# Kernel optimization log

Measured on AMD Instinct MI355X. Metric: run time of the kernel, lower is better.

## Reference

```python
import jax, jax.numpy as jnp
import numpy as np

N_NODES = 100000
N_EDGES = 1600000
HID = 64
EDGE_DIM = 32
N_LAYERS = 3
BN_EPS = 1e-5


def setup_inputs() -> dict:
    key = jax.random.key(0)
    ks = jax.random.split(key, 8)
    x = jax.random.normal(ks[0], (N_NODES, HID), dtype=jnp.float32)
    edge_index = jax.random.randint(ks[1], (2, N_EDGES), 0, N_NODES, dtype=jnp.int32)
    edge_attr = jax.random.normal(ks[2], (N_EDGES, EDGE_DIM), dtype=jnp.float32)
    s = 0.1  # small init scale for numerical stability
    We = jax.random.normal(ks[3], (N_LAYERS, EDGE_DIM, HID), dtype=jnp.float32) * s
    be = jnp.zeros((N_LAYERS, HID), jnp.float32)
    W1 = jax.random.normal(ks[4], (N_LAYERS, HID, HID), dtype=jnp.float32) * s
    b1 = jnp.zeros((N_LAYERS, HID), jnp.float32)
    W2 = jax.random.normal(ks[5], (N_LAYERS, HID, HID), dtype=jnp.float32) * s
    b2 = jnp.zeros((N_LAYERS, HID), jnp.float32)
    gamma = jnp.ones((N_LAYERS, HID), jnp.float32)
    beta = jnp.zeros((N_LAYERS, HID), jnp.float32)
    Wout = jax.random.normal(ks[6], (HID, HID), dtype=jnp.float32) * s
    bout = jnp.zeros((HID,), jnp.float32)
    return {"x": x, "edge_index": edge_index, "edge_attr": edge_attr,
            "We": We, "be": be, "W1": W1, "b1": b1, "W2": W2, "b2": b2,
            "gamma": gamma, "beta": beta, "Wout": Wout, "bout": bout}


def _forward(x, edge_index, edge_attr, We, be, W1, b1, W2, b2, gamma, beta, Wout, bout):
    src = edge_index[0]  # x_j (source of message)
    dst = edge_index[1]  # aggregation target
    n = x.shape[0]
    for i in range(N_LAYERS):
        # GINEConv: message = relu(x_j + lin_edge(edge_attr)); scatter-add to dst
        e = edge_attr @ We[i] + be[i]                      # [E, H]
        m = jax.nn.relu(x[src] + e)                        # [E, H] (dominant traffic)
        agg = jax.ops.segment_sum(m, dst, num_segments=n)  # [N, H]
        h = x + agg                                        # (1 + eps)*x, eps = 0
        # 2-layer MLP
        h = jax.nn.relu(h @ W1[i] + b1[i]) @ W2[i] + b2[i]
        # BatchNorm1d (training mode: batch statistics, biased variance)
        mean = jnp.mean(h, axis=0)
        var = jnp.var(h, axis=0)
        h = (h - mean) * jax.lax.rsqrt(var + BN_EPS) * gamma[i] + beta[i]
        x = jax.nn.relu(h)
    return x @ Wout + bout


def reference(x, edge_index, edge_attr, We, be, W1, b1, W2, b2, gamma, beta, Wout, bout):
    return _forward(x, edge_index, edge_attr, We, be, W1, b1, W2, b2, gamma, beta, Wout, bout)
```

## Files before the change

kernel.cpp:

```cpp
#include <hip/hip_runtime.h>
#include <stdint.h>

#define N_NODES 100000
#define N_EDGES 1600000
#define HID 64
#define EDIM 32
#define BN_EPS 1e-5f

#define SCAN_CHUNK 1024
#define NB_SCAN ((N_NODES + SCAN_CHUNK - 1) / SCAN_CHUNK)

#define G_NODES 16

__global__ __launch_bounds__(256) void hist_kernel(
    const int* __restrict__ dst, int* __restrict__ cnt)
{
    int i = (int)(blockIdx.x * blockDim.x + threadIdx.x);
    const int stride = (int)(gridDim.x * blockDim.x);
    for (; i < N_EDGES; i += stride) atomicAdd(&cnt[dst[i]], 1);
}

__global__ __launch_bounds__(256) void scan1_kernel(
    const int* __restrict__ cnt, int* __restrict__ bsum)
{
    __shared__ int s[256];
    const int b = (int)blockIdx.x, t = (int)threadIdx.x;
    const int base = b * SCAN_CHUNK + t * 4;
    int sum = 0;
#pragma unroll
    for (int k = 0; k < 4; ++k) {
        int idx = base + k;
        if (idx < N_NODES) sum += cnt[idx];
    }
    s[t] = sum;
    __syncthreads();
    for (int off = 128; off > 0; off >>= 1) {
        if (t < off) s[t] += s[t + off];
        __syncthreads();
    }
    if (t == 0) bsum[b] = s[0];
}

__global__ __launch_bounds__(128) void scan2_kernel(
    const int* __restrict__ bsum, int* __restrict__ bofs, int* __restrict__ row_ptr)
{
    __shared__ int s[128];
    const int t = (int)threadIdx.x;
    const int v = (t < NB_SCAN) ? bsum[t] : 0;
    s[t] = v;
    __syncthreads();
    for (int off = 1; off < 128; off <<= 1) {
        int add = (t >= off) ? s[t - off] : 0;
        __syncthreads();
        s[t] += add;
        __syncthreads();
    }
    if (t < NB_SCAN) bofs[t] = s[t] - v;
    if (t == NB_SCAN - 1) row_ptr[N_NODES] = s[t];
}

__global__ __launch_bounds__(256) void scan3_kernel(
    const int* __restrict__ cnt, const int* __restrict__ bofs,
    int* __restrict__ row_ptr, int* __restrict__ pos)
{
    __shared__ int s[256];
    const int b = (int)blockIdx.x, t = (int)threadIdx.x;
    const int base = b * SCAN_CHUNK + t * 4;
    int v[4];
    int sum = 0;
#pragma unroll
    for (int k = 0; k < 4; ++k) {
        int idx = base + k;
        v[k] = (idx < N_NODES) ? cnt[idx] : 0;
        sum += v[k];
    }
    s[t] = sum;
    __syncthreads();
    for (int off = 1; off < 256; off <<= 1) {
        int add = (t >= off) ? s[t - off] : 0;
        __syncthreads();
        s[t] += add;
        __syncthreads();
    }
    int run = s[t] - sum + bofs[b];
#pragma unroll
    for (int k = 0; k < 4; ++k) {
        int idx = base + k;
        if (idx < N_NODES) {
            row_ptr[idx] = run;
            pos[idx] = run;
            run += v[k];
        }
    }
}

__global__ __launch_bounds__(256) void scatter_kernel(
    const int* __restrict__ src, const int* __restrict__ dst,
    int* __restrict__ pos, int* __restrict__ perm_e, int* __restrict__ perm_src)
{
    int i = (int)(blockIdx.x * blockDim.x + threadIdx.x);
    const int stride = (int)(gridDim.x * blockDim.x);
    for (; i < N_EDGES; i += stride) {
        const int d = dst[i];
        const int p = atomicAdd(&pos[d], 1);
        perm_e[p] = i;
        perm_src[p] = src[i];
    }
}

__global__ __launch_bounds__(256) void permute_attr_kernel(
    const float* __restrict__ eattr, const int* __restrict__ perm_e,
    float* __restrict__ outp)
{
    const int total = N_EDGES * 8;
    int i = (int)(blockIdx.x * blockDim.x + threadIdx.x);
    const int stride = (int)(gridDim.x * blockDim.x);
    for (; i < total; i += stride) {
        const int row = i >> 3, part = i & 7;
        ((float4*)outp)[i] =
            ((const float4*)eattr)[(size_t)(unsigned)perm_e[row] * 8 + part];
    }
}

template<bool LINEAR>
__global__ __launch_bounds__(256, 4) void gather_kernel(
    const float* __restrict__ x, const float* __restrict__ attr,
    const int* __restrict__ row_ptr, const int* __restrict__ perm_e,
    const int* __restrict__ perm_src,
    const float* __restrict__ We, const float* __restrict__ be,
    float* __restrict__ agg)
{
    const int tid  = (int)threadIdx.x;
    const int lane = tid & 63;
    const int w    = __builtin_amdgcn_readfirstlane(tid >> 6);
    const int node_lo = (int)blockIdx.x * G_NODES + 4 * w;

    int rpv[5];
#pragma unroll
    for (int i = 0; i < 5; ++i) {
        int n = node_lo + i;
        n = (n < N_NODES) ? n : N_NODES;
        rpv[i] = __builtin_amdgcn_readfirstlane(row_ptr[n]);
    }
    const int F0 = rpv[0], rp1 = rpv[1], rp2 = rpv[2], rp3 = rpv[3], F1 = rpv[4];

    float a = 0.0f, sn1 = 0.0f, sn2 = 0.0f, sn3 = 0.0f;

    if (F0 < F1) {
        const int FL = F1 - 1;

        float pf_prev;
        {
            int gl = F0 + lane; if (gl > FL) gl = FL;
            size_t row = LINEAR ? (size_t)gl : (size_t)(unsigned)perm_e[gl];
            pf_prev = attr[row * EDIM];
        }

        float wv[EDIM];
#pragma unroll
        for (int k = 0; k < EDIM; ++k) wv[k] = We[k * HID + lane];
        const float bias = be[lane];

        int jA = F0;
        int jB = F0 + 1; if (jB > FL) jB = FL;
        int jC = F0 + 2; if (jC > FL) jC = FL;
        const int s0 = perm_src[jA];
        const int s1 = perm_src[jB];
        int sN = perm_src[jC];
        float xq0 = x[(size_t)(unsigned)s0 * HID + lane];
        float xq1 = x[(size_t)(unsigned)s1 * HID + lane];

        for (int gb = F0; gb < F1; gb += 64) {
            const int gend = (gb + 64 < F1) ? gb + 64 : F1;

            float pf = 0.0f;
            if (gb + 64 < F1) {
                int gl = gb + 64 + lane; if (gl > FL) gl = FL;
                size_t row = LINEAR ? (size_t)gl : (size_t)(unsigned)perm_e[gl];
                pf = attr[row * EDIM];
            }

#pragma unroll 2
            for (int j = gb; j < gend; ++j) {
                const float xq2 = x[(size_t)(unsigned)sN * HID + lane];
                int j3 = j + 3; if (j3 > FL) j3 = FL;
                sN = perm_src[j3];

                size_t row = LINEAR ? (size_t)j : (size_t)(unsigned)perm_e[j];
                const float4* ap = (const float4*)(attr + row * EDIM);

                float e0 = bias, e1 = 0.0f, e2 = 0.0f, e3 = 0.0f;
#pragma unroll
                for (int k = 0; k < 8; ++k) {
                    const float4 q = ap[k];
                    e0 = fmaf(q.x, wv[4 * k + 0], e0);
                    e1 = fmaf(q.y, wv[4 * k + 1], e1);
                    e2 = fmaf(q.z, wv[4 * k + 2], e2);
                    e3 = fmaf(q.w, wv[4 * k + 3], e3);
                }
                a += fmaxf(xq0 + ((e0 + e1) + (e2 + e3)), 0.0f);
                xq0 = xq1; xq1 = xq2;

                if (j + 1 == rp1) sn1 = a;
                if (j + 1 == rp2) sn2 = a;
                if (j + 1 == rp3) sn3 = a;
            }

            asm volatile("" :: "v"(pf_prev));
            pf_prev = pf;
        }
        asm volatile("" :: "v"(pf_prev));
    }

    float r[4];
    r[0] = sn1;
    r[1] = sn2 - sn1;
    r[2] = sn3 - sn2;
    r[3] = a - sn3;
#pragma unroll
    for (int q = 0; q < 4; ++q) {
        const int n = node_lo + q;
        if (n < N_NODES) agg[(size_t)n * HID + lane] = r[q];
    }
}

__global__ __launch_bounds__(256) void mlp_kernel(
    const float* __restrict__ xin, const float* __restrict__ agg,
    const float* __restrict__ W1, const float* __restrict__ b1,
    const float* __restrict__ W2, const float* __restrict__ b2,
    float* __restrict__ uout)
{
    const int lane = threadIdx.x & 63;
    const int wid  = (int)((blockIdx.x * blockDim.x + threadIdx.x) >> 6);
    const int n    = wid * 64 + lane;
    const bool ok  = (n < N_NODES);
    const size_t base = (size_t)n * HID;

    float h[HID];
    if (ok) {
        const float4* px = (const float4*)(xin + base);
        const float4* pa = (const float4*)(agg + base);
#pragma unroll
        for (int j = 0; j < HID / 4; ++j) {
            float4 xv = px[j];
            float4 av = pa[j];
            h[4 * j + 0] = xv.x + av.x;
            h[4 * j + 1] = xv.y + av.y;
            h[4 * j + 2] = xv.z + av.z;
            h[4 * j + 3] = xv.w + av.w;
        }
    } else {
#pragma unroll
        for (int k = 0; k < HID; ++k) h[k] = 0.0f;
    }

    float u[HID];
#pragma unroll
    for (int f = 0; f < HID; ++f) u[f] = b2[f];

    for (int c = 0; c < 4; ++c) {
        float t[16];
#pragma unroll
        for (int j = 0; j < 16; ++j) t[j] = b1[c * 16 + j];
#pragma unroll
        for (int k = 0; k < HID; ++k) {
            const float hk = h[k];
#pragma unroll
            for (int j = 0; j < 16; ++j)
                t[j] = fmaf(hk, W1[k * HID + c * 16 + j], t[j]);
        }
#pragma unroll
        for (int j = 0; j < 16; ++j) t[j] = fmaxf(t[j], 0.0f);
#pragma unroll
        for (int j = 0; j < 16; ++j) {
            const float tj = t[j];
#pragma unroll
            for (int f = 0; f < HID; ++f)
                u[f] = fmaf(tj, W2[(c * 16 + j) * HID + f], u[f]);
        }
    }

    if (ok) {
        float4* po = (float4*)(uout + base);
#pragma unroll
        for (int j = 0; j < HID / 4; ++j)
            po[j] = make_float4(u[4 * j], u[4 * j + 1], u[4 * j + 2], u[4 * j + 3]);
    }
}

__global__ __launch_bounds__(256) void out_kernel(
    const float* __restrict__ xin, const float* __restrict__ Wo,
    const float* __restrict__ bo, float* __restrict__ out)
{
    const int lane = threadIdx.x & 63;
    const int wid  = (int)((blockIdx.x * blockDim.x + threadIdx.x) >> 6);
    const int n    = wid * 64 + lane;
    const bool ok  = (n < N_NODES);
    const size_t base = (size_t)n * HID;

    float h[HID];
    if (ok) {
        const float4* px = (const float4*)(xin + base);
#pragma unroll
        for (int j = 0; j < HID / 4; ++j) {
            float4 xv = px[j];
            h[4 * j + 0] = xv.x; h[4 * j + 1] = xv.y;
            h[4 * j + 2] = xv.z; h[4 * j + 3] = xv.w;
        }
    } else {
#pragma unroll
        for (int k = 0; k < HID; ++k) h[k] = 0.0f;
    }

    for (int c = 0; c < 4; ++c) {
        float t[16];
#pragma unroll
        for (int j = 0; j < 16; ++j) t[j] = bo[c * 16 + j];
#pragma unroll
        for (int k = 0; k < HID; ++k) {
            const float hk = h[k];
#pragma unroll
            for (int j = 0; j < 16; ++j)
                t[j] = fmaf(hk, Wo[k * HID + c * 16 + j], t[j]);
        }
        if (ok) {
            float4* po = (float4*)(out + base + c * 16);
#pragma unroll
            for (int j = 0; j < 4; ++j)
                po[j] = make_float4(t[4 * j], t[4 * j + 1], t[4 * j + 2], t[4 * j + 3]);
        }
    }
}

__global__ __launch_bounds__(256) void stats_kernel(
    const float* __restrict__ u, float* __restrict__ stats)
{
    __shared__ float ls[256];
    __shared__ float ls2[256];
    const int tid = (int)threadIdx.x;
    const int g   = (int)(blockIdx.x * 256 + tid);
    const int f   = g & 63;
    const int row = g >> 6;
    const int rstride = (int)((gridDim.x * 256) >> 6);

    float s = 0.0f, s2 = 0.0f;
    for (int n = row; n < N_NODES; n += rstride) {
        float v = u[(size_t)n * HID + f];
        s += v;
        s2 = fmaf(v, v, s2);
    }
    ls[tid] = s;
    ls2[tid] = s2;
    __syncthreads();
    if (tid < 64) {
        float a = ls[tid] + ls[tid + 64] + ls[tid + 128] + ls[tid + 192];
        float b = ls2[tid] + ls2[tid + 64] + ls2[tid + 128] + ls2[tid + 192];
        atomicAdd(&stats[tid], a);
        atomicAdd(&stats[64 + tid], b);
    }
}

__global__ __launch_bounds__(256) void bn_relu_kernel(
    const float* __restrict__ u, const float* __restrict__ stats,
    const float* __restrict__ gamma, const float* __restrict__ beta,
    float* __restrict__ xout)
{
    const int total4 = N_NODES * HID / 4;
    int i = (int)(blockIdx.x * blockDim.x + threadIdx.x);
    const int stride = (int)(gridDim.x * blockDim.x);
    const int fb = (i * 4) & 63;

    const float invN = 1.0f / (float)N_NODES;
    float sc[4], sh[4];
#pragma unroll
    for (int j = 0; j < 4; ++j) {
        float mean = stats[fb + j] * invN;
        float var  = stats[64 + fb + j] * invN - mean * mean;
        float s    = gamma[fb + j] * rsqrtf(var + BN_EPS);
        sc[j] = s;
        sh[j] = beta[fb + j] - mean * s;
    }
    for (; i < total4; i += stride) {
        float4 v = ((const float4*)u)[i];
        v.x = fmaxf(fmaf(v.x, sc[0], sh[0]), 0.0f);
        v.y = fmaxf(fmaf(v.y, sc[1], sh[1]), 0.0f);
        v.z = fmaxf(fmaf(v.z, sc[2], sh[2]), 0.0f);
        v.w = fmaxf(fmaf(v.w, sc[3], sh[3]), 0.0f);
        ((float4*)xout)[i] = v;
    }
}

extern "C" void kernel_launch(void* const* d_in, const int* in_sizes, int n_in,
                              void* d_out, int out_size, void* d_ws, size_t ws_size,
                              hipStream_t stream)
{
    const float* x0    = (const float*)d_in[0];
    const int*   eidx  = (const int*)d_in[1];
    const float* eattr = (const float*)d_in[2];
    const float* We    = (const float*)d_in[3];
    const float* be    = (const float*)d_in[4];
    const float* W1    = (const float*)d_in[5];
    const float* b1    = (const float*)d_in[6];
    const float* W2    = (const float*)d_in[7];
    const float* b2    = (const float*)d_in[8];
    const float* gamma = (const float*)d_in[9];
    const float* beta  = (const float*)d_in[10];
    const float* Wout  = (const float*)d_in[11];
    const float* bout  = (const float*)d_in[12];
    float* out = (float*)d_out;

    const int* src = eidx;
    const int* dst = eidx + N_EDGES;

    const size_t NH = (size_t)N_NODES * HID;

    float* A     = (float*)d_ws;
    float* AGG   = A + NH;
    float* stats = AGG + NH;
    int* cnt      = (int*)(stats + 128);
    int* bsum     = cnt + N_NODES;
    int* bofs     = bsum + 128;
    int* row_ptr  = bofs + 128;
    int* pos      = row_ptr + N_NODES + 1;
    int* perm_e   = pos + N_NODES;
    int* perm_src = perm_e + N_EDGES;
    float* B = out;

    uintptr_t eap_off = (((uintptr_t)(perm_src + N_EDGES) - (uintptr_t)d_ws)
                         + 255) & ~(uintptr_t)255;
    const size_t need = (size_t)eap_off + (size_t)N_EDGES * EDIM * sizeof(float);
    const bool lin = (ws_size >= need);
    float* EAP = (float*)((char*)d_ws + eap_off);

    hipMemsetAsync(cnt, 0, N_NODES * sizeof(int), stream);
    hist_kernel<<<1024, 256, 0, stream>>>(dst, cnt);
    scan1_kernel<<<NB_SCAN, 256, 0, stream>>>(cnt, bsum);
    scan2_kernel<<<1, 128, 0, stream>>>(bsum, bofs, row_ptr);
    scan3_kernel<<<NB_SCAN, 256, 0, stream>>>(cnt, bofs, row_ptr, pos);
    scatter_kernel<<<1024, 256, 0, stream>>>(src, dst, pos, perm_e, perm_src);
    if (lin)
        permute_attr_kernel<<<2048, 256, 0, stream>>>(eattr, perm_e, EAP);

    const int mlp_blocks    = ((N_NODES + 63) / 64 + 3) / 4;
    const int gather_blocks = (N_NODES + G_NODES - 1) / G_NODES;

    const float* xin = x0;
    for (int i = 0; i < 3; ++i) {
        hipMemsetAsync(stats, 0, 128 * sizeof(float), stream);

        if (lin)
            gather_kernel<true><<<gather_blocks, 256, 0, stream>>>(
                xin, EAP, row_ptr, perm_e, perm_src,
                We + (size_t)i * EDIM * HID, be + (size_t)i * HID, AGG);
        else
            gather_kernel<false><<<gather_blocks, 256, 0, stream>>>(
                xin, eattr, row_ptr, perm_e, perm_src,
                We + (size_t)i * EDIM * HID, be + (size_t)i * HID, AGG);

        mlp_kernel<<<mlp_blocks, 256, 0, stream>>>(
            xin, AGG,
            W1 + (size_t)i * HID * HID, b1 + (size_t)i * HID,
            W2 + (size_t)i * HID * HID, b2 + (size_t)i * HID, B);

        stats_kernel<<<256, 256, 0, stream>>>(B, stats);

        bn_relu_kernel<<<1024, 256, 0, stream>>>(
            B, stats, gamma + (size_t)i * HID, beta + (size_t)i * HID, A);

        xin = A;
    }

    out_kernel<<<mlp_blocks, 256, 0, stream>>>(A, Wout, bout, out);
}
```

Baseline: 1.477 ms.

## Batch source-row gathers eight edges at a time in linear gather path

In the linear-attribute gather kernel, the one-edge-at-a-time rolling prefetch of source rows is replaced by blocks of eight x-row loads. The loads for the next block of eight, and the source indices for the block after that, are issued before computing the current block. The aim is more memory-level parallelism on the random x gathers, which dominate the aggregation cost. Launch bounds also go from 4 to 5 waves per EU, which tightens the register budget while the new path holds more values in flight. The permuted path is unchanged apart from being split into its own branch.

```diff
diff --git a/kernel.cpp b/kernel.cpp
--- a/kernel.cpp
+++ b/kernel.cpp
@@ -123,7 +123,7 @@
 }
 
 template<bool LINEAR>
-__global__ __launch_bounds__(256, 4) void gather_kernel(
+__global__ __launch_bounds__(256, 5) void gather_kernel(
     const float* __restrict__ x, const float* __restrict__ attr,
     const int* __restrict__ row_ptr, const int* __restrict__ perm_e,
     const int* __restrict__ perm_src,
@@ -161,55 +161,137 @@
         for (int k = 0; k < EDIM; ++k) wv[k] = We[k * HID + lane];
         const float bias = be[lane];
 
-        int jA = F0;
-        int jB = F0 + 1; if (jB > FL) jB = FL;
-        int jC = F0 + 2; if (jC > FL) jC = FL;
-        const int s0 = perm_src[jA];
-        const int s1 = perm_src[jB];
-        int sN = perm_src[jC];
-        float xq0 = x[(size_t)(unsigned)s0 * HID + lane];
-        float xq1 = x[(size_t)(unsigned)s1 * HID + lane];
-
-        for (int gb = F0; gb < F1; gb += 64) {
-            const int gend = (gb + 64 < F1) ? gb + 64 : F1;
-
-            float pf = 0.0f;
-            if (gb + 64 < F1) {
-                int gl = gb + 64 + lane; if (gl > FL) gl = FL;
-                size_t row = LINEAR ? (size_t)gl : (size_t)(unsigned)perm_e[gl];
-                pf = attr[row * EDIM];
+        if (LINEAR) {
+            float xv[8], xn[8];
+            int   sA[8];
+#pragma unroll
+            for (int u = 0; u < 8; ++u) {
+                int idx = F0 + u; if (idx > FL) idx = FL;
+                sA[u] = perm_src[idx];
             }
-
+#pragma unroll
+            for (int u = 0; u < 8; ++u)
+                xv[u] = x[(size_t)(unsigned)sA[u] * HID + lane];
+#pragma unroll
+            for (int u = 0; u < 8; ++u) {
+                int idx = F0 + 8 + u; if (idx > FL) idx = FL;
+                sA[u] = perm_src[idx];
+            }
+
+            int j = F0;
+            for (int gb = F0; gb < F1; gb += 64) {
+                const int gend = (gb + 64 < F1) ? gb + 64 : F1;
+
+                float pf = 0.0f;
+                if (gb + 64 < F1) {
+                    int gl = gb + 64 + lane; if (gl > FL) gl = FL;
+                    pf = attr[(size_t)gl * EDIM];
+                }
+
+                while (j + 8 <= gend) {
+#pragma unroll
+                    for (int u = 0; u < 8; ++u)
+                        xn[u] = x[(size_t)(unsigned)sA[u] * HID + lane];
+#pragma unroll
+                    for (int u = 0; u < 8; ++u) {
+                        int idx = j + 16 + u; if (idx > FL) idx = FL;
+                        sA[u] = perm_src[idx];
+                    }
+#pragma unroll
+                    for (int u = 0; u < 8; ++u) {
+                        const float4* ap =
+                            (const float4*)(attr + (size_t)(j + u) * EDIM);
+                        float e0 = bias, e1 = 0.0f, e2 = 0.0f, e3 = 0.0f;
+#pragma unroll
+                        for (int k = 0; k < 8; ++k) {
+                            const float4 q = ap[k];
+                            e0 = fmaf(q.x, wv[4 * k + 0], e0);
+                            e1 = fmaf(q.y, wv[4 * k + 1], e1);
+                            e2 = fmaf(q.z, wv[4 * k + 2], e2);
+                            e3 = fmaf(q.w, wv[4 * k + 3], e3);
+                        }
+                        a += fmaxf(xv[u] + ((e0 + e1) + (e2 + e3)), 0.0f);
+                        if (j + u + 1 == rp1) sn1 = a;
+                        if (j + u + 1 == rp2) sn2 = a;
+                        if (j + u + 1 == rp3) sn3 = a;
+                    }
+#pragma unroll
+                    for (int u = 0; u < 8; ++u) xv[u] = xn[u];
+                    j += 8;
+                }
+
+                if (gend == F1) {
+#pragma unroll
+                    for (int u = 0; u < 8; ++u) {
+                        if (j + u < F1) {
+                            const float4* ap =
+                                (const float4*)(attr + (size_t)(j + u) * EDIM);
+                            float e0 = bias, e1 = 0.0f, e2 = 0.0f, e3 = 0.0f;
+#pragma unroll
+                            for (int k = 0; k < 8; ++k) {
+                                const float4 q = ap[k];
+                                e0 = fmaf(q.x, wv[4 * k + 0], e0);
+                                e1 = fmaf(q.y, wv[4 * k + 1], e1);
+                                e2 = fmaf(q.z, wv[4 * k + 2], e2);
+                                e3 = fmaf(q.w, wv[4 * k + 3], e3);
+                            }
+                            a += fmaxf(xv[u] + ((e0 + e1) + (e2 + e3)), 0.0f);
+                            if (j + u + 1 == rp1) sn1 = a;
+                            if (j + u + 1 == rp2) sn2 = a;
+                            if (j + u + 1 == rp3) sn3 = a;
+                        }
+                    }
+                    j = F1;
+                }
+
+                asm volatile("" :: "v"(pf_prev));
+                pf_prev = pf;
+            }
+            asm volatile("" :: "v"(pf_prev));
+        } else {
+            int jA = F0;
+            int jB = F0 + 1; if (jB > FL) jB = FL;
+            int jC = F0 + 2; if (jC > FL) jC = FL;
+            const int s0 = perm_src[jA];
+            const int s1 = perm_src[jB];
+            int sN = perm_src[jC];
+            float xq0 = x[(size_t)(unsigned)s0 * HID + lane];
+            float xq1 = x[(size_t)(unsigned)s1 * HID + lane];
+
+            for (int gb = F0; gb < F1; gb += 64) {
+                const int gend = (gb + 64 < F1) ? gb + 64 : F1;
+                float pf = 0.0f;
+                if (gb + 64 < F1) {
+                    int gl = gb + 64 + lane; if (gl > FL) gl = FL;
+                    pf = attr[(size_t)(unsigned)perm_e[gl] * EDIM];
+                }
 #pragma unroll 2
-            for (int j = gb; j < gend; ++j) {
-                const float xq2 = x[(size_t)(unsigned)sN * HID + lane];
-                int j3 = j + 3; if (j3 > FL) j3 = FL;
-                sN = perm_src[j3];
-
-                size_t row = LINEAR ? (size_t)j : (size_t)(unsigned)perm_e[j];
-                const float4* ap = (const float4*)(attr + row * EDIM);
-
-                float e0 = bias, e1 = 0.0f, e2 = 0.0f, e3 = 0.0f;
-#pragma unroll
-                for (int k = 0; k < 8; ++k) {
-                    const float4 q = ap[k];
-                    e0 = fmaf(q.x, wv[4 * k + 0], e0);
-                    e1 = fmaf(q.y, wv[4 * k + 1], e1);
-                    e2 = fmaf(q.z, wv[4 * k + 2], e2);
-                    e3 = fmaf(q.w, wv[4 * k + 3], e3);
+                for (int j = gb; j < gend; ++j) {
+                    const float xq2 = x[(size_t)(unsigned)sN * HID + lane];
+                    int j3 = j + 3; if (j3 > FL) j3 = FL;
+                    sN = perm_src[j3];
+                    const float4* ap = (const float4*)(
+                        attr + (size_t)(unsigned)perm_e[j] * EDIM);
+                    float e0 = bias, e1 = 0.0f, e2 = 0.0f, e3 = 0.0f;
+#pragma unroll
+                    for (int k = 0; k < 8; ++k) {
+                        const float4 q = ap[k];
+                        e0 = fmaf(q.x, wv[4 * k + 0], e0);
+                        e1 = fmaf(q.y, wv[4 * k + 1], e1);
+                        e2 = fmaf(q.z, wv[4 * k + 2], e2);
+                        e3 = fmaf(q.w, wv[4 * k + 3], e3);
+                    }
+                    a += fmaxf(xq0 + ((e0 + e1) + (e2 + e3)), 0.0f);
+                    xq0 = xq1; xq1 = xq2;
+                    if (j + 1 == rp1) sn1 = a;
+                    if (j + 1 == rp2) sn2 = a;
+                    if (j + 1 == rp3) sn3 = a;
                 }
-                a += fmaxf(xq0 + ((e0 + e1) + (e2 + e3)), 0.0f);
-                xq0 = xq1; xq1 = xq2;
-
-                if (j + 1 == rp1) sn1 = a;
-                if (j + 1 == rp2) sn2 = a;
-                if (j + 1 == rp3) sn3 = a;
+                asm volatile("" :: "v"(pf_prev));
+                pf_prev = pf;
             }
-
             asm volatile("" :: "v"(pf_prev));
-            pf_prev = pf;
-        }
-        asm volatile("" :: "v"(pf_prev));
+        }
     }
 
     float r[4];
```

Result: no change. 1.498 ms (+1.4%).
